# Kernel optimization log

Measured on AMD Instinct MI355X. Metric: run time of the kernel, lower is better.

## Reference

```python
import jax, jax.numpy as jnp
import numpy as np

MAX_FRAMES = 12
TOPK = 49
NUM_SAMPLES = 256
SIGMA = 0.05
LN_EPS = 1e-5


def setup_inputs() -> dict:
    key = jax.random.key(0)
    ks = jax.random.split(key, 6)
    B, MF, N, D = 8, MAX_FRAMES, 197, 512
    x = jax.random.normal(ks[0], (B, MF * N, D), dtype=jnp.float32)
    noise = jax.random.normal(ks[1], (B * MF, NUM_SAMPLES, N - 1), dtype=jnp.float32)
    ln_gamma = jnp.ones((D,), jnp.float32)
    ln_beta = jnp.zeros((D,), jnp.float32)
    w_in = jax.random.normal(ks[2], (D, D // 2), dtype=jnp.float32) * 0.02
    w1 = jax.random.normal(ks[3], (D, D // 2), dtype=jnp.float32) * 0.02
    w2 = jax.random.normal(ks[4], (D // 2, 1), dtype=jnp.float32) * 0.02
    return {"x": x, "noise": noise, "ln_gamma": ln_gamma, "ln_beta": ln_beta,
            "w_in": w_in, "w1": w1, "w2": w2}


def reference(x, noise, ln_gamma, ln_beta, w_in, w1, w2):
    B, L, D = x.shape
    N = L // MAX_FRAMES
    xf = x.reshape(B * MAX_FRAMES, N, D)          # (b, N, D)

    # PredictorLG: LayerNorm -> Linear -> GELU (torch GELU is exact erf)
    mu = xf.mean(-1, keepdims=True)
    var = xf.var(-1, keepdims=True)               # biased, matches torch LayerNorm
    hn = (xf - mu) * jax.lax.rsqrt(var + LN_EPS) * ln_gamma + ln_beta
    h = jax.nn.gelu(hn @ w_in, approximate=False)  # (b, N, D/2)
    # concat local features with broadcast global (cls-token) features
    g = jnp.broadcast_to(h[:, :1, :], h.shape)
    cat = jnp.concatenate([h, g], axis=-1)         # (b, N, D)
    score = jnp.tanh(jax.nn.gelu(cat @ w1, approximate=False) @ w2)[..., 0]  # (b, N)

    sp = score[:, 1:]                              # (b, d) spatial scores, d = N-1
    b_eff, ns, d = noise.shape
    pert = sp[:, None, :] + noise * SIGMA          # (b, ns, d)

    # top-k set per sample; sorted ascending (matches torch sort of topk indices)
    order = jnp.argsort(-pert, axis=-1)            # descending by value
    top_sorted = jnp.sort(order[..., :TOPK], axis=-1)  # (b, ns, k)

    # mean of one-hots == scatter-add counts / num_samples (avoids one-hot blowup)
    bi = jnp.arange(b_eff)[:, None, None]
    pos = jnp.arange(TOPK)[None, None, :]
    ind = jnp.zeros((b_eff, TOPK, d), x.dtype).at[bi, pos, top_sorted].add(1.0) / ns

    cls_feat = xf[:, :1, :]                        # (b, 1, D)
    spat_feat = xf[:, 1:, :]                       # (b, d, D)
    sel = jnp.einsum('bkl,bld->bkd', ind, spat_feat)  # (b, k, D)
    out = jnp.concatenate([cls_feat, sel], axis=1)    # (b, 1+k, D)
    return out.reshape(B, MAX_FRAMES * (1 + TOPK), D)
```

## Files before the change

kernel.cpp:

```cpp
#include <hip/hip_runtime.h>
#include <math.h>

#define NFRAME 96
#define NTOK   197
#define NSPAT  196
#define DIM    512
#define DH     256
#define NSAMP  256
#define KSEL   49
#define SIG    0.05f
#define MPAD   208
#define MTOT   (NFRAME * MPAD)
#define HSEG   (KSEL * NSPAT)

typedef unsigned short u16;
typedef __attribute__((ext_vector_type(8))) short bf16x8;
typedef __attribute__((ext_vector_type(4))) float f32x4;

__device__ __forceinline__ float gelu_exact(float v) {
    return 0.5f * v * (1.0f + erff(v * 0.70710678118654752440f));
}
__device__ __forceinline__ unsigned bf16_rne(float f) {
    unsigned u = __float_as_uint(f);
    return (u + 0x7fffu + ((u >> 16) & 1u)) >> 16;
}
__device__ __forceinline__ float bf16_to_f(unsigned h) {
    return __uint_as_float(h << 16);
}

__device__ __forceinline__ void gld16(const u16* g, u16* l) {
    __builtin_amdgcn_global_load_lds(
        (const __attribute__((address_space(1))) void*)g,
        (__attribute__((address_space(3))) void*)l, 16, 0, 0);
}
__device__ __forceinline__ bf16x8 srd(const u16* base, int r, int cw) {
    return *(const bf16x8*)((const char*)base + r * 128 + (((cw) ^ (r & 7)) << 4));
}

__global__ __launch_bounds__(256) void k0_prep(
    const float* __restrict__ x, const float* __restrict__ gamma,
    const float* __restrict__ beta,
    const float* __restrict__ w_in, const float* __restrict__ w1,
    u16* __restrict__ wiT_hi, u16* __restrict__ wiT_lo,
    u16* __restrict__ w1T_hi, u16* __restrict__ w1T_lo,
    u16* __restrict__ xs_hi, u16* __restrict__ xs_lo)
{
    if (blockIdx.x < 512) {
        const int n = blockIdx.x & 255, which = blockIdx.x >> 8;
        const float* w = which ? w1 : w_in;
        u16* th = which ? w1T_hi : wiT_hi;
        u16* tl = which ? w1T_lo : wiT_lo;
        for (int k = threadIdx.x; k < DIM; k += 256) {
            float v = w[(size_t)k * DH + n];
            unsigned hi = bf16_rne(v);
            unsigned lo = bf16_rne(v - bf16_to_f(hi));
            th[(size_t)n * DIM + k] = (u16)hi;
            tl[(size_t)n * DIM + k] = (u16)lo;
        }
        return;
    }
    const int row  = (blockIdx.x - 512) * 4 + (threadIdx.x >> 6);
    const int lane = threadIdx.x & 63;
    const int f = row / MPAD;
    int rr = row - f * MPAD; if (rr > NTOK - 1) rr = NTOK - 1;
    const float* xr = x + ((size_t)f * NTOK + rr) * DIM + lane * 8;
    float4 a = *(const float4*)xr, b4 = *(const float4*)(xr + 4);
    float e[8] = {a.x, a.y, a.z, a.w, b4.x, b4.y, b4.z, b4.w};
    float s = 0.f, sq = 0.f;
    #pragma unroll
    for (int j = 0; j < 8; ++j) { s += e[j]; sq += e[j] * e[j]; }
    #pragma unroll
    for (int o = 32; o > 0; o >>= 1) {
        s  += __shfl_xor(s,  o, 64);
        sq += __shfl_xor(sq, o, 64);
    }
    const float mu  = s * (1.f / 512.f);
    const float var = sq * (1.f / 512.f) - mu * mu;
    const float rs  = 1.f / sqrtf(var + 1e-5f);

    const float* gp = gamma + lane * 8;
    const float* bp = beta + lane * 8;
    float4 g0 = *(const float4*)gp, g1 = *(const float4*)(gp + 4);
    float4 b0 = *(const float4*)bp, b1 = *(const float4*)(bp + 4);
    float gg[8] = {g0.x, g0.y, g0.z, g0.w, g1.x, g1.y, g1.z, g1.w};
    float bt[8] = {b0.x, b0.y, b0.z, b0.w, b1.x, b1.y, b1.z, b1.w};

    unsigned hw[4], lw[4];
    #pragma unroll
    for (int p = 0; p < 4; ++p) {
        float s0 = rs * gg[2*p],   s1 = rs * gg[2*p+1];
        float v0 = e[2*p]   * s0 + (bt[2*p]   - mu * s0);
        float v1 = e[2*p+1] * s1 + (bt[2*p+1] - mu * s1);
        unsigned h0 = bf16_rne(v0), h1 = bf16_rne(v1);
        float l0 = v0 - bf16_to_f(h0), l1 = v1 - bf16_to_f(h1);
        hw[p] = h0 | (h1 << 16);
        lw[p] = bf16_rne(l0) | (bf16_rne(l1) << 16);
    }
    size_t off = (size_t)row * DIM + lane * 8;
    *(uint4*)(xs_hi + off) = make_uint4(hw[0], hw[1], hw[2], hw[3]);
    *(uint4*)(xs_lo + off) = make_uint4(lw[0], lw[1], lw[2], lw[3]);
}

__global__ __launch_bounds__(256, 3) void k1_gemm1(
    const u16* __restrict__ xs_hi, const u16* __restrict__ xs_lo,
    const u16* __restrict__ wiT_hi, const u16* __restrict__ wiT_lo,
    u16* __restrict__ h_hi, u16* __restrict__ h_lo)
{
    __shared__ u16 Ah[128][64], Al[128][64], Bh[64][64], Bl[64][64];
    const int t = threadIdx.x, lane = t & 63, wv = t >> 6;
    const int linear = (blockIdx.x & 7) * 78 + (blockIdx.x >> 3);
    const int Mb = linear >> 2, Nb = linear & 3;
    const int R0 = Mb * 128, N0 = Nb * 64;
    const int wm = wv >> 1, wn = wv & 1;
    const int m15 = lane & 15, q = lane >> 4;
    const int r8 = lane >> 3;
    const int cg = (lane & 7) ^ r8;

    f32x4 acc[4][2];
    #pragma unroll
    for (int i = 0; i < 4; ++i)
        #pragma unroll
        for (int j = 0; j < 2; ++j)
            acc[i][j] = (f32x4){0.f, 0.f, 0.f, 0.f};

    for (int k0 = 0; k0 < DIM; k0 += 64) {
        __syncthreads();
        #pragma unroll
        for (int j = 0; j < 4; ++j) {
            const int rA = wv * 32 + j * 8;
            const size_t src = (size_t)(R0 + rA + r8) * DIM + k0 + cg * 8;
            gld16(xs_hi + src, &Ah[rA][0]);
            gld16(xs_lo + src, &Al[rA][0]);
        }
        #pragma unroll
        for (int j = 0; j < 2; ++j) {
            const int rB = wv * 16 + j * 8;
            const size_t src = (size_t)(N0 + rB + r8) * DIM + k0 + cg * 8;
            gld16(wiT_hi + src, &Bh[rB][0]);
            gld16(wiT_lo + src, &Bl[rB][0]);
        }
        __syncthreads();

        #pragma unroll
        for (int kh = 0; kh < 2; ++kh) {
            const int cw = kh * 4 + q;
            bf16x8 a_h[4], a_l[4], b_h[2], b_l[2];
            #pragma unroll
            for (int i = 0; i < 4; ++i) {
                const int r = wm * 64 + i * 16 + m15;
                a_h[i] = srd(&Ah[0][0], r, cw);
                a_l[i] = srd(&Al[0][0], r, cw);
            }
            #pragma unroll
            for (int n = 0; n < 2; ++n) {
                const int r = wn * 32 + n * 16 + m15;
                b_h[n] = srd(&Bh[0][0], r, cw);
                b_l[n] = srd(&Bl[0][0], r, cw);
            }
            #pragma unroll
            for (int mt = 0; mt < 4; ++mt)
                #pragma unroll
                for (int nt = 0; nt < 2; ++nt) {
                    f32x4 c = acc[mt][nt];
                    c = __builtin_amdgcn_mfma_f32_16x16x32_bf16(a_h[mt], b_h[nt], c, 0, 0, 0);
                    c = __builtin_amdgcn_mfma_f32_16x16x32_bf16(a_l[mt], b_h[nt], c, 0, 0, 0);
                    c = __builtin_amdgcn_mfma_f32_16x16x32_bf16(a_h[mt], b_l[nt], c, 0, 0, 0);
                    acc[mt][nt] = c;
                }
        }
    }

    #pragma unroll
    for (int mt = 0; mt < 4; ++mt)
        #pragma unroll
        for (int nt = 0; nt < 2; ++nt)
            #pragma unroll
            for (int reg = 0; reg < 4; ++reg) {
                int r = R0 + wm*64 + mt*16 + q*4 + reg;
                int c = N0 + wn*32 + nt*16 + m15;
                float v = gelu_exact(acc[mt][nt][reg]);
                unsigned hb = bf16_rne(v);
                unsigned lb = bf16_rne(v - bf16_to_f(hb));
                size_t off = (size_t)r * DH + c;
                h_hi[off] = (u16)hb;
                h_lo[off] = (u16)lb;
            }
}

__global__ __launch_bounds__(256) void k1g_gbias(
    const u16* __restrict__ h_hi, const u16* __restrict__ h_lo,
    const u16* __restrict__ w1T_hi, const u16* __restrict__ w1T_lo,
    float* __restrict__ gbias)
{
    const int f = blockIdx.x, n = threadIdx.x;
    const size_t hoff = (size_t)f * MPAD * DH;
    const size_t woff = (size_t)n * DIM + DH;
    float s = 0.f;
    for (int k = 0; k < DH; k += 8) {
        uint4 vh = *(const uint4*)(h_hi + hoff + k);
        uint4 vl = *(const uint4*)(h_lo + hoff + k);
        uint4 uh = *(const uint4*)(w1T_hi + woff + k);
        uint4 ul = *(const uint4*)(w1T_lo + woff + k);
        const unsigned* ph = (const unsigned*)&vh;
        const unsigned* pl = (const unsigned*)&vl;
        const unsigned* qh = (const unsigned*)&uh;
        const unsigned* ql = (const unsigned*)&ul;
        #pragma unroll
        for (int w = 0; w < 4; ++w) {
            float a0 = bf16_to_f(ph[w] & 0xffffu) + bf16_to_f(pl[w] & 0xffffu);
            float a1 = bf16_to_f(ph[w] >> 16)     + bf16_to_f(pl[w] >> 16);
            float b0 = bf16_to_f(qh[w] & 0xffffu) + bf16_to_f(ql[w] & 0xffffu);
            float b1 = bf16_to_f(qh[w] >> 16)     + bf16_to_f(ql[w] >> 16);
            s += a0 * b0 + a1 * b1;
        }
    }
    gbias[f * DH + n] = s;
}

__global__ __launch_bounds__(256, 3) void k1_gemm2(
    const u16* __restrict__ h_hi, const u16* __restrict__ h_lo,
    const u16* __restrict__ w1T_hi, const u16* __restrict__ w1T_lo,
    const float* __restrict__ w2, const float* __restrict__ gbias,
    float* __restrict__ s_quar)
{
    __shared__ u16 Ah[128][64], Al[128][64], Bh[64][64], Bl[64][64];
    __shared__ float red[2][2][64];
    const int t = threadIdx.x, lane = t & 63, wv = t >> 6;
    const int linear = (blockIdx.x & 7) * 78 + (blockIdx.x >> 3);
    const int Mb = linear >> 2, Nb = linear & 3;
    const int R0 = Mb * 128, N0 = Nb * 64;
    const int wm = wv >> 1, wn = wv & 1;
    const int m15 = lane & 15, q = lane >> 4;
    const int r8 = lane >> 3;
    const int cg = (lane & 7) ^ r8;

    f32x4 acc[4][2];
    #pragma unroll
    for (int i = 0; i < 4; ++i)
        #pragma unroll
        for (int j = 0; j < 2; ++j)
            acc[i][j] = (f32x4){0.f, 0.f, 0.f, 0.f};

    for (int k0 = 0; k0 < DH; k0 += 64) {
        __syncthreads();
        #pragma unroll
        for (int j = 0; j < 4; ++j) {
            const int rA = wv * 32 + j * 8;
            const size_t src = (size_t)(R0 + rA + r8) * DH + k0 + cg * 8;
            gld16(h_hi + src, &Ah[rA][0]);
            gld16(h_lo + src, &Al[rA][0]);
        }
        #pragma unroll
        for (int j = 0; j < 2; ++j) {
            const int rB = wv * 16 + j * 8;
            const size_t src = (size_t)(N0 + rB + r8) * DIM + k0 + cg * 8;
            gld16(w1T_hi + src, &Bh[rB][0]);
            gld16(w1T_lo + src, &Bl[rB][0]);
        }
        __syncthreads();

        #pragma unroll
        for (int kh = 0; kh < 2; ++kh) {
            const int cw = kh * 4 + q;
            bf16x8 a_h[4], a_l[4], b_h[2], b_l[2];
            #pragma unroll
            for (int i = 0; i < 4; ++i) {
                const int r = wm * 64 + i * 16 + m15;
                a_h[i] = srd(&Ah[0][0], r, cw);
                a_l[i] = srd(&Al[0][0], r, cw);
            }
            #pragma unroll
            for (int n = 0; n < 2; ++n) {
                const int r = wn * 32 + n * 16 + m15;
                b_h[n] = srd(&Bh[0][0], r, cw);
                b_l[n] = srd(&Bl[0][0], r, cw);
            }
            #pragma unroll
            for (int mt = 0; mt < 4; ++mt)
                #pragma unroll
                for (int nt = 0; nt < 2; ++nt) {
                    f32x4 c = acc[mt][nt];
                    c = __builtin_amdgcn_mfma_f32_16x16x32_bf16(a_h[mt], b_h[nt], c, 0, 0, 0);
                    c = __builtin_amdgcn_mfma_f32_16x16x32_bf16(a_l[mt], b_h[nt], c, 0, 0, 0);
                    c = __builtin_amdgcn_mfma_f32_16x16x32_bf16(a_h[mt], b_l[nt], c, 0, 0, 0);
                    acc[mt][nt] = c;
                }
        }
    }

    float w2v[2];
    int   cIdx[2];
    #pragma unroll
    for (int nt = 0; nt < 2; ++nt) {
        cIdx[nt] = N0 + wn*32 + nt*16 + m15;
        w2v[nt]  = w2[cIdx[nt]];
    }
    #pragma unroll
    for (int mt = 0; mt < 4; ++mt)
        #pragma unroll
        for (int reg = 0; reg < 4; ++reg) {
            int r = R0 + wm*64 + mt*16 + q*4 + reg;
            int f = r / MPAD;
            float gb0 = gbias[f * DH + cIdx[0]];
            float gb1 = gbias[f * DH + cIdx[1]];
            float s = gelu_exact(acc[mt][0][reg] + gb0) * w2v[0] +
                      gelu_exact(acc[mt][1][reg] + gb1) * w2v[1];
            #pragma unroll
            for (int o = 1; o <= 8; o <<= 1)
                s += __shfl_xor(s, o, 64);
            if (m15 == 0)
                red[wn][wm][mt*16 + q*4 + reg] = s;
        }
    __syncthreads();
    if (t < 128) {
        int wmj = t >> 6, rl = t & 63;
        float sv = red[0][wmj][rl] + red[1][wmj][rl];
        s_quar[(size_t)Nb * MTOT + R0 + t] = sv;
    }
}

__global__ __launch_bounds__(1024) void k2_select(
    const float* __restrict__ s_quar, const float* __restrict__ noise,
    u16* __restrict__ hist2)
{
    const int fb   = blockIdx.x;
    const int f    = fb >> 2;
    const int qt   = fb & 3;
    const int t    = threadIdx.x;
    const int lane = t & 63;
    const int wv   = t >> 6;

    __shared__ int hist_s[HSEG];
    for (int i = t; i < HSEG; i += 1024) hist_s[i] = 0;

    const float* s0 = s_quar;
    const float* s1 = s_quar + MTOT;
    const float* s2 = s_quar + 2 * (size_t)MTOT;
    const float* s3 = s_quar + 3 * (size_t)MTOT;
    float spv[4];
    #pragma unroll
    for (int j = 0; j < 4; ++j) {
        int l = lane + 64 * j;
        if (l < NSPAT) {
            size_t idx = (size_t)f * MPAD + 1 + l;
            spv[j] = tanhf(s0[idx] + s1[idx] + s2[idx] + s3[idx]);
        } else spv[j] = 0.f;
    }
    __syncthreads();

    const unsigned long long lmask = (1ull << lane) - 1ull;

    for (int si = 0; si < 4; ++si) {
        const int s = qt * 64 + wv * 4 + si;
        const float* nz = noise + ((size_t)f * NSAMP + s) * NSPAT;
        unsigned key[4];
        #pragma unroll
        for (int j = 0; j < 4; ++j) {
            int l = lane + 64 * j;
            if (l < NSPAT) {
                float p = spv[j] + nz[l] * SIG;
                unsigned u = __float_as_uint(p);
                key[j] = (u & 0x80000000u) ? ~u : (u | 0x80000000u);
            } else {
                key[j] = 0u;
            }
        }

        unsigned ans;
        int c31 = 0;
        {
            #pragma unroll
            for (int j = 0; j < 4; ++j)
                c31 += __popcll(__ballot(key[j] >= 0x80000000u));
            ans = (c31 >= KSEL) ? 0x80000000u : 0x40000000u;
        }
        if (c31 != KSEL) {
            for (int bit = 29; bit >= 0; --bit) {
                unsigned cand = ans | (1u << bit);
                int cnt = 0;
                #pragma unroll
                for (int j = 0; j < 4; ++j)
                    cnt += __popcll(__ballot(key[j] >= cand));
                if (cnt >= KSEL) {
                    ans = cand;
                    if (cnt == KSEL) break;
                }
            }
        }

        unsigned long long eq[4];
        int cgt = 0;
        #pragma unroll
        for (int j = 0; j < 4; ++j) {
            cgt += __popcll(__ballot(key[j] > ans));
            eq[j] = __ballot(key[j] == ans);
        }
        const int quota = KSEL - cgt;
        int eqpre[4]; { int run = 0;
            #pragma unroll
            for (int j = 0; j < 4; ++j) { eqpre[j] = run; run += __popcll(eq[j]); } }

        int pre = 0;
        #pragma unroll
        for (int j = 0; j < 4; ++j) {
            bool iseq = (key[j] == ans);
            int trk = eqpre[j] + __popcll(eq[j] & lmask);
            bool selj = (key[j] > ans) || (iseq && trk < quota);
            unsigned long long sb = __ballot(selj);
            int rk = pre + __popcll(sb & lmask);
            if (selj)
                atomicAdd(&hist_s[rk * NSPAT + lane + 64 * j], 1);
            pre += __popcll(sb);
        }
    }

    __syncthreads();
    u16* hb = hist2 + (size_t)fb * HSEG;
    for (int i = t; i < HSEG; i += 1024)
        hb[i] = (u16)hist_s[i];
}

#define KP3 52
__global__ __launch_bounds__(256) void k3_output(
    const float* __restrict__ x, const u16* __restrict__ hist2,
    float* __restrict__ out)
{
    const int b   = blockIdx.x >> 3;
    const int ds  = blockIdx.x & 7;
    const int d0  = ds * 64;
    const int t   = threadIdx.x;
    const int tdc = t & 15;
    const int tk  = t >> 4;

    __shared__ float hist_s[NSPAT * KP3 + 16];

    const u16* hbase = hist2 + (size_t)(4 * b) * HSEG;
    for (int i = t; i < HSEG; i += 256) {
        int k = i / NSPAT;
        int l = i - k * NSPAT;
        int sum = (int)hbase[i] + (int)hbase[i + HSEG]
                + (int)hbase[i + 2 * HSEG] + (int)hbase[i + 3 * HSEG];
        hist_s[l * KP3 + k] = (float)sum;
    }
    for (int i = t; i < NSPAT * 3 + 16; i += 256) {
        int l = i / 3, j = i - l * 3;
        int idx = (i < NSPAT * 3) ? (l * KP3 + KSEL + j) : (NSPAT * KP3 + i - NSPAT * 3);
        hist_s[idx] = 0.f;
    }
    if (t < 64)
        out[(size_t)b * 50 * DIM + d0 + t] = x[(size_t)b * NTOK * DIM + d0 + t];
    __syncthreads();

    const float* xs = x + ((size_t)b * NTOK + 1) * DIM + d0 + tdc * 4;
    float4 acc[4];
    #pragma unroll
    for (int i = 0; i < 4; ++i) acc[i] = make_float4(0.f, 0.f, 0.f, 0.f);

    #pragma unroll 7
    for (int l = 0; l < NSPAT; ++l) {
        float4 v  = *(const float4*)(xs + (size_t)l * DIM);
        float4 w4 = *(const float4*)&hist_s[l * KP3 + tk * 4];
        acc[0].x += w4.x * v.x; acc[0].y += w4.x * v.y;
        acc[0].z += w4.x * v.z; acc[0].w += w4.x * v.w;
        acc[1].x += w4.y * v.x; acc[1].y += w4.y * v.y;
        acc[1].z += w4.y * v.z; acc[1].w += w4.y * v.w;
        acc[2].x += w4.z * v.x; acc[2].y += w4.z * v.y;
        acc[2].z += w4.z * v.z; acc[2].w += w4.z * v.w;
        acc[3].x += w4.w * v.x; acc[3].y += w4.w * v.y;
        acc[3].z += w4.w * v.z; acc[3].w += w4.w * v.w;
    }

    const float inv = 1.f / 256.f;
    #pragma unroll
    for (int i = 0; i < 4; ++i) {
        int k = tk * 4 + i;
        if (k < KSEL) {
            float4 o = make_float4(acc[i].x * inv, acc[i].y * inv,
                                   acc[i].z * inv, acc[i].w * inv);
            *(float4*)&out[((size_t)b * 50 + 1 + k) * DIM + d0 + tdc * 4] = o;
        }
    }
}

extern "C" void kernel_launch(void* const* d_in, const int* in_sizes, int n_in,
                              void* d_out, int out_size, void* d_ws, size_t ws_size,
                              hipStream_t stream)
{
    const float* x     = (const float*)d_in[0];
    const float* noise = (const float*)d_in[1];
    const float* gamma = (const float*)d_in[2];
    const float* beta  = (const float*)d_in[3];
    const float* w_in  = (const float*)d_in[4];
    const float* w1    = (const float*)d_in[5];
    const float* w2    = (const float*)d_in[6];
    float* out = (float*)d_out;

    char* ws = (char*)d_ws;
    u16*   hist2   = (u16*)  (ws + 0);
    float* gbias   = (float*)(ws + 0);
    float* s_quar  = (float*)(ws + 7375872);
    u16*   wiT_hi  = (u16*)  (ws + 7695360);
    u16*   wiT_lo  = (u16*)  (ws + 7957504);
    u16*   w1T_hi  = (u16*)  (ws + 8219648);
    u16*   w1T_lo  = (u16*)  (ws + 8481792);
    u16*   h_hi    = (u16*)  (ws + 8743936);
    u16*   h_lo    = (u16*)  (ws + 18967552);
    u16*   xs_hi   = (u16*)  (ws + 29191168);
    u16*   xs_lo   = (u16*)  (ws + 49638400);

    k0_prep<<<512 + MTOT / 4, 256, 0, stream>>>(x, gamma, beta, w_in, w1,
                                                wiT_hi, wiT_lo, w1T_hi, w1T_lo,
                                                xs_hi, xs_lo);
    k1_gemm1<<<(MTOT / 128) * 4, 256, 0, stream>>>(xs_hi, xs_lo, wiT_hi, wiT_lo,
                                                   h_hi, h_lo);
    k1g_gbias<<<NFRAME, 256, 0, stream>>>(h_hi, h_lo, w1T_hi, w1T_lo, gbias);
    k1_gemm2<<<(MTOT / 128) * 4, 256, 0, stream>>>(h_hi, h_lo, w1T_hi, w1T_lo,
                                                   w2, gbias, s_quar);
    k2_select<<<NFRAME * 4, 1024, 0, stream>>>(s_quar, noise, hist2);
    k3_output<<<NFRAME * 8, 256, 0, stream>>>(x, hist2, out);
}
```

Measured before the change: 198.9 us.

## Shrink GEMM M-tile to 64 rows and assign one operand per wave for loads

Both split-bf16 GEMM kernels now use 64x64 output tiles instead of 128x64, doubling the grid and halving per-block LDS and accumulator registers so more blocks can be resident (launch bounds raised). Global-to-LDS staging is restructured so each wave loads one whole operand buffer (A-hi, A-lo, B-hi, B-lo). The intent is better occupancy and wave balance across the GPU for these mid-size GEMMs. In exchange, B tiles are reloaded twice as often and arithmetic intensity per block drops.

```diff
diff --git a/kernel.cpp b/kernel.cpp
--- a/kernel.cpp
+++ b/kernel.cpp
@@ -101,24 +101,30 @@
     *(uint4*)(xs_lo + off) = make_uint4(lw[0], lw[1], lw[2], lw[3]);
 }
 
-__global__ __launch_bounds__(256, 3) void k1_gemm1(
+__global__ __launch_bounds__(256, 5) void k1_gemm1(
     const u16* __restrict__ xs_hi, const u16* __restrict__ xs_lo,
     const u16* __restrict__ wiT_hi, const u16* __restrict__ wiT_lo,
     u16* __restrict__ h_hi, u16* __restrict__ h_lo)
 {
-    __shared__ u16 Ah[128][64], Al[128][64], Bh[64][64], Bl[64][64];
+    __shared__ u16 Ah[64][64], Al[64][64], Bh[64][64], Bl[64][64];
     const int t = threadIdx.x, lane = t & 63, wv = t >> 6;
-    const int linear = (blockIdx.x & 7) * 78 + (blockIdx.x >> 3);
+    const int linear = (blockIdx.x & 7) * 156 + (blockIdx.x >> 3);
     const int Mb = linear >> 2, Nb = linear & 3;
-    const int R0 = Mb * 128, N0 = Nb * 64;
+    const int R0 = Mb * 64, N0 = Nb * 64;
     const int wm = wv >> 1, wn = wv & 1;
     const int m15 = lane & 15, q = lane >> 4;
     const int r8 = lane >> 3;
     const int cg = (lane & 7) ^ r8;
 
-    f32x4 acc[4][2];
-    #pragma unroll
-    for (int i = 0; i < 4; ++i)
+    const u16* gsrc = (wv == 0) ? xs_hi : (wv == 1) ? xs_lo
+                    : (wv == 2) ? wiT_hi : wiT_lo;
+    u16* ldst = (wv == 0) ? &Ah[0][0] : (wv == 1) ? &Al[0][0]
+              : (wv == 2) ? &Bh[0][0] : &Bl[0][0];
+    const int rbase = (wv < 2) ? R0 : N0;
+
+    f32x4 acc[2][2];
+    #pragma unroll
+    for (int i = 0; i < 2; ++i)
         #pragma unroll
         for (int j = 0; j < 2; ++j)
             acc[i][j] = (f32x4){0.f, 0.f, 0.f, 0.f};
@@ -126,57 +132,46 @@
     for (int k0 = 0; k0 < DIM; k0 += 64) {
         __syncthreads();
         #pragma unroll
-        for (int j = 0; j < 4; ++j) {
-            const int rA = wv * 32 + j * 8;
-            const size_t src = (size_t)(R0 + rA + r8) * DIM + k0 + cg * 8;
-            gld16(xs_hi + src, &Ah[rA][0]);
-            gld16(xs_lo + src, &Al[rA][0]);
-        }
-        #pragma unroll
-        for (int j = 0; j < 2; ++j) {
-            const int rB = wv * 16 + j * 8;
-            const size_t src = (size_t)(N0 + rB + r8) * DIM + k0 + cg * 8;
-            gld16(wiT_hi + src, &Bh[rB][0]);
-            gld16(wiT_lo + src, &Bl[rB][0]);
+        for (int j = 0; j < 8; ++j) {
+            const int rr = j * 8;
+            const size_t src = (size_t)(rbase + rr + r8) * DIM + k0 + cg * 8;
+            gld16(gsrc + src, ldst + rr * 64);
         }
         __syncthreads();
 
         #pragma unroll
         for (int kh = 0; kh < 2; ++kh) {
             const int cw = kh * 4 + q;
-            bf16x8 a_h[4], a_l[4], b_h[2], b_l[2];
-            #pragma unroll
-            for (int i = 0; i < 4; ++i) {
-                const int r = wm * 64 + i * 16 + m15;
-                a_h[i] = srd(&Ah[0][0], r, cw);
-                a_l[i] = srd(&Al[0][0], r, cw);
+            bf16x8 ah[2], al[2], bh[2], bl[2];
+            #pragma unroll
+            for (int i = 0; i < 2; ++i) {
+                const int ra = wm * 32 + i * 16 + m15;
+                const int rb = wn * 32 + i * 16 + m15;
+                ah[i] = srd(&Ah[0][0], ra, cw);
+                al[i] = srd(&Al[0][0], ra, cw);
+                bh[i] = srd(&Bh[0][0], rb, cw);
+                bl[i] = srd(&Bl[0][0], rb, cw);
             }
             #pragma unroll
-            for (int n = 0; n < 2; ++n) {
-                const int r = wn * 32 + n * 16 + m15;
-                b_h[n] = srd(&Bh[0][0], r, cw);
-                b_l[n] = srd(&Bl[0][0], r, cw);
-            }
-            #pragma unroll
-            for (int mt = 0; mt < 4; ++mt)
+            for (int mt = 0; mt < 2; ++mt)
                 #pragma unroll
                 for (int nt = 0; nt < 2; ++nt) {
                     f32x4 c = acc[mt][nt];
-                    c = __builtin_amdgcn_mfma_f32_16x16x32_bf16(a_h[mt], b_h[nt], c, 0, 0, 0);
-                    c = __builtin_amdgcn_mfma_f32_16x16x32_bf16(a_l[mt], b_h[nt], c, 0, 0, 0);
-                    c = __builtin_amdgcn_mfma_f32_16x16x32_bf16(a_h[mt], b_l[nt], c, 0, 0, 0);
+                    c = __builtin_amdgcn_mfma_f32_16x16x32_bf16(ah[mt], bh[nt], c, 0, 0, 0);
+                    c = __builtin_amdgcn_mfma_f32_16x16x32_bf16(al[mt], bh[nt], c, 0, 0, 0);
+                    c = __builtin_amdgcn_mfma_f32_16x16x32_bf16(ah[mt], bl[nt], c, 0, 0, 0);
                     acc[mt][nt] = c;
                 }
         }
     }
 
     #pragma unroll
-    for (int mt = 0; mt < 4; ++mt)
+    for (int mt = 0; mt < 2; ++mt)
         #pragma unroll
         for (int nt = 0; nt < 2; ++nt)
             #pragma unroll
             for (int reg = 0; reg < 4; ++reg) {
-                int r = R0 + wm*64 + mt*16 + q*4 + reg;
+                int r = R0 + wm*32 + mt*16 + q*4 + reg;
                 int c = N0 + wn*32 + nt*16 + m15;
                 float v = gelu_exact(acc[mt][nt][reg]);
                 unsigned hb = bf16_rne(v);
@@ -217,26 +212,33 @@
     gbias[f * DH + n] = s;
 }
 
-__global__ __launch_bounds__(256, 3) void k1_gemm2(
+__global__ __launch_bounds__(256, 4) void k1_gemm2(
     const u16* __restrict__ h_hi, const u16* __restrict__ h_lo,
     const u16* __restrict__ w1T_hi, const u16* __restrict__ w1T_lo,
     const float* __restrict__ w2, const float* __restrict__ gbias,
     float* __restrict__ s_quar)
 {
-    __shared__ u16 Ah[128][64], Al[128][64], Bh[64][64], Bl[64][64];
-    __shared__ float red[2][2][64];
+    __shared__ u16 Ah[64][64], Al[64][64], Bh[64][64], Bl[64][64];
+    __shared__ float red[2][2][32];
     const int t = threadIdx.x, lane = t & 63, wv = t >> 6;
-    const int linear = (blockIdx.x & 7) * 78 + (blockIdx.x >> 3);
+    const int linear = (blockIdx.x & 7) * 156 + (blockIdx.x >> 3);
     const int Mb = linear >> 2, Nb = linear & 3;
-    const int R0 = Mb * 128, N0 = Nb * 64;
+    const int R0 = Mb * 64, N0 = Nb * 64;
     const int wm = wv >> 1, wn = wv & 1;
     const int m15 = lane & 15, q = lane >> 4;
     const int r8 = lane >> 3;
     const int cg = (lane & 7) ^ r8;
 
-    f32x4 acc[4][2];
-    #pragma unroll
-    for (int i = 0; i < 4; ++i)
+    const u16* gsrc = (wv == 0) ? h_hi : (wv == 1) ? h_lo
+                    : (wv == 2) ? w1T_hi : w1T_lo;
+    u16* ldst = (wv == 0) ? &Ah[0][0] : (wv == 1) ? &Al[0][0]
+              : (wv == 2) ? &Bh[0][0] : &Bl[0][0];
+    const int rbase = (wv < 2) ? R0 : N0;
+    const size_t rstride = (wv < 2) ? DH : DIM;
+
+    f32x4 acc[2][2];
+    #pragma unroll
+    for (int i = 0; i < 2; ++i)
         #pragma unroll
         for (int j = 0; j < 2; ++j)
             acc[i][j] = (f32x4){0.f, 0.f, 0.f, 0.f};
@@ -244,45 +246,34 @@
     for (int k0 = 0; k0 < DH; k0 += 64) {
         __syncthreads();
         #pragma unroll
-        for (int j = 0; j < 4; ++j) {
-            const int rA = wv * 32 + j * 8;
-            const size_t src = (size_t)(R0 + rA + r8) * DH + k0 + cg * 8;
-            gld16(h_hi + src, &Ah[rA][0]);
-            gld16(h_lo + src, &Al[rA][0]);
-        }
-        #pragma unroll
-        for (int j = 0; j < 2; ++j) {
-            const int rB = wv * 16 + j * 8;
-            const size_t src = (size_t)(N0 + rB + r8) * DIM + k0 + cg * 8;
-            gld16(w1T_hi + src, &Bh[rB][0]);
-            gld16(w1T_lo + src, &Bl[rB][0]);
+        for (int j = 0; j < 8; ++j) {
+            const int rr = j * 8;
+            const size_t src = (size_t)(rbase + rr + r8) * rstride + k0 + cg * 8;
+            gld16(gsrc + src, ldst + rr * 64);
         }
         __syncthreads();
 
         #pragma unroll
         for (int kh = 0; kh < 2; ++kh) {
             const int cw = kh * 4 + q;
-            bf16x8 a_h[4], a_l[4], b_h[2], b_l[2];
-            #pragma unroll
-            for (int i = 0; i < 4; ++i) {
-                const int r = wm * 64 + i * 16 + m15;
-                a_h[i] = srd(&Ah[0][0], r, cw);
-                a_l[i] = srd(&Al[0][0], r, cw);
+            bf16x8 ah[2], al[2], bh[2], bl[2];
+            #pragma unroll
+            for (int i = 0; i < 2; ++i) {
+                const int ra = wm * 32 + i * 16 + m15;
+                const int rb = wn * 32 + i * 16 + m15;
+                ah[i] = srd(&Ah[0][0], ra, cw);
+                al[i] = srd(&Al[0][0], ra, cw);
+                bh[i] = srd(&Bh[0][0], rb, cw);
+                bl[i] = srd(&Bl[0][0], rb, cw);
             }
             #pragma unroll
-            for (int n = 0; n < 2; ++n) {
-                const int r = wn * 32 + n * 16 + m15;
-                b_h[n] = srd(&Bh[0][0], r, cw);
-                b_l[n] = srd(&Bl[0][0], r, cw);
-            }
-            #pragma unroll
-            for (int mt = 0; mt < 4; ++mt)
+            for (int mt = 0; mt < 2; ++mt)
                 #pragma unroll
                 for (int nt = 0; nt < 2; ++nt) {
                     f32x4 c = acc[mt][nt];
-                    c = __builtin_amdgcn_mfma_f32_16x16x32_bf16(a_h[mt], b_h[nt], c, 0, 0, 0);
-                    c = __builtin_amdgcn_mfma_f32_16x16x32_bf16(a_l[mt], b_h[nt], c, 0, 0, 0);
-                    c = __builtin_amdgcn_mfma_f32_16x16x32_bf16(a_h[mt], b_l[nt], c, 0, 0, 0);
+                    c = __builtin_amdgcn_mfma_f32_16x16x32_bf16(ah[mt], bh[nt], c, 0, 0, 0);
+                    c = __builtin_amdgcn_mfma_f32_16x16x32_bf16(al[mt], bh[nt], c, 0, 0, 0);
+                    c = __builtin_amdgcn_mfma_f32_16x16x32_bf16(ah[mt], bl[nt], c, 0, 0, 0);
                     acc[mt][nt] = c;
                 }
         }
@@ -296,10 +287,10 @@
         w2v[nt]  = w2[cIdx[nt]];
     }
     #pragma unroll
-    for (int mt = 0; mt < 4; ++mt)
+    for (int mt = 0; mt < 2; ++mt)
         #pragma unroll
         for (int reg = 0; reg < 4; ++reg) {
-            int r = R0 + wm*64 + mt*16 + q*4 + reg;
+            int r = R0 + wm*32 + mt*16 + q*4 + reg;
             int f = r / MPAD;
             float gb0 = gbias[f * DH + cIdx[0]];
             float gb1 = gbias[f * DH + cIdx[1]];
@@ -312,8 +303,8 @@
                 red[wn][wm][mt*16 + q*4 + reg] = s;
         }
     __syncthreads();
-    if (t < 128) {
-        int wmj = t >> 6, rl = t & 63;
+    if (t < 64) {
+        int wmj = t >> 5, rl = t & 31;
         float sv = red[0][wmj][rl] + red[1][wmj][rl];
         s_quar[(size_t)Nb * MTOT + R0 + t] = sv;
     }
@@ -511,11 +502,11 @@
     k0_prep<<<512 + MTOT / 4, 256, 0, stream>>>(x, gamma, beta, w_in, w1,
                                                 wiT_hi, wiT_lo, w1T_hi, w1T_lo,
                                                 xs_hi, xs_lo);
-    k1_gemm1<<<(MTOT / 128) * 4, 256, 0, stream>>>(xs_hi, xs_lo, wiT_hi, wiT_lo,
-                                                   h_hi, h_lo);
+    k1_gemm1<<<(MTOT / 64) * 4, 256, 0, stream>>>(xs_hi, xs_lo, wiT_hi, wiT_lo,
+                                                  h_hi, h_lo);
     k1g_gbias<<<NFRAME, 256, 0, stream>>>(h_hi, h_lo, w1T_hi, w1T_lo, gbias);
-    k1_gemm2<<<(MTOT / 128) * 4, 256, 0, stream>>>(h_hi, h_lo, w1T_hi, w1T_lo,
-                                                   w2, gbias, s_quar);
+    k1_gemm2<<<(MTOT / 64) * 4, 256, 0, stream>>>(h_hi, h_lo, w1T_hi, w1T_lo,
+                                                  w2, gbias, s_quar);
     k2_select<<<NFRAME * 4, 1024, 0, stream>>>(s_quar, noise, hist2);
     k3_output<<<NFRAME * 8, 256, 0, stream>>>(x, hist2, out);
 }
```

Measured after the change: 204.4 us. +2.8%, slower.
